# Kernel tuning notes

Hardware: AMD Instinct MI355X
Metric: run time of the kernel (lower is better)

## Reference

```python
import jax, jax.numpy as jnp
import numpy as np

VOCAB, EMB, HID, T = 33, 16, 128, 14

def setup_inputs() -> dict:
    key = jax.random.key(0)
    ks = jax.random.split(key, 12)
    B = 131072
    x = jax.random.randint(ks[0], (B, T), 0, VOCAB, dtype=jnp.int32)
    s = 1.0 / np.sqrt(HID)
    emb_table = jax.random.normal(ks[1], (VOCAB, EMB), dtype=jnp.float32)
    # torch LSTM params: gate order [i, f, g, o], uniform(-1/sqrt(H), 1/sqrt(H))
    W_ih = jax.random.uniform(ks[2], (4 * HID, EMB), minval=-s, maxval=s, dtype=jnp.float32)
    W_hh = jax.random.uniform(ks[3], (4 * HID, HID), minval=-s, maxval=s, dtype=jnp.float32)
    b_ih = jax.random.uniform(ks[4], (4 * HID,), minval=-s, maxval=s, dtype=jnp.float32)
    b_hh = jax.random.uniform(ks[5], (4 * HID,), minval=-s, maxval=s, dtype=jnp.float32)
    W1 = jax.random.uniform(ks[6], (64, 128), minval=-s, maxval=s, dtype=jnp.float32)
    b1 = jax.random.uniform(ks[7], (64,), minval=-s, maxval=s, dtype=jnp.float32)
    W2 = jax.random.uniform(ks[8], (32, 64), minval=-0.125, maxval=0.125, dtype=jnp.float32)
    b2 = jax.random.uniform(ks[9], (32,), minval=-0.125, maxval=0.125, dtype=jnp.float32)
    W3 = jax.random.uniform(ks[10], (2, 32), minval=-0.176, maxval=0.176, dtype=jnp.float32)
    b3 = jax.random.uniform(ks[11], (2,), minval=-0.176, maxval=0.176, dtype=jnp.float32)
    return {"x": x, "emb_table": emb_table, "W_ih": W_ih, "W_hh": W_hh,
            "b_ih": b_ih, "b_hh": b_hh, "W1": W1, "b1": b1,
            "W2": W2, "b2": b2, "W3": W3, "b3": b3}

def reference(x, emb_table, W_ih, W_hh, b_ih, b_hh, W1, b1, W2, b2, W3, b3):
    B = x.shape[0]
    # padding_idx=0: row 0 is zero
    table = emb_table.at[0].set(0.0)
    emb = table[x]                                # [B, T, E]
    # precompute input projections for all timesteps in one GEMM
    x_proj = jnp.einsum('bte,ge->btg', emb, W_ih) + b_ih + b_hh  # [B, T, 4H]

    def step(carry, xp_t):
        h, c = carry
        gates = xp_t + h @ W_hh.T                 # [B, 4H]
        i, f, g, o = jnp.split(gates, 4, axis=-1)
        i, f, o = jax.nn.sigmoid(i), jax.nn.sigmoid(f), jax.nn.sigmoid(o)
        g = jnp.tanh(g)
        c = f * c + i * g
        h = o * jnp.tanh(c)
        return (h, c), None

    h0 = jnp.zeros((B, HID), dtype=emb.dtype)
    c0 = jnp.zeros((B, HID), dtype=emb.dtype)
    (h_last, _), _ = jax.lax.scan(step, (h0, c0), jnp.swapaxes(x_proj, 0, 1))

    y = jax.nn.sigmoid(h_last @ W1.T + b1)
    y = jax.nn.sigmoid(y @ W2.T + b2)
    return y @ W3.T + b3                          # [B, 2]
```

## Files before the change

### kernel.cpp

```cpp
#include <hip/hip_runtime.h>
#include <hip/hip_bf16.h>

#define TSTEP 14
#define BROWS 128
#define KCOMB 160
#define ESTR  16
#define L2E   1.4426950408889634f
#define L2E2  2.8853900817779268f

typedef __attribute__((ext_vector_type(8))) short bf16x8;
typedef __attribute__((ext_vector_type(4))) float f32x4;
typedef __attribute__((ext_vector_type(4))) int   i32x4;

#define MFMA(a,b,c) __builtin_amdgcn_mfma_f32_16x16x32_bf16((a),(b),(c),0,0,0)

__device__ inline ushort f2b(float f){
  union { float f; unsigned u; } v; v.f = f;
  unsigned r = v.u + 0x7fff + ((v.u >> 16) & 1);
  return (ushort)(r >> 16);
}
__device__ inline float rcpf(float x){ return __builtin_amdgcn_rcpf(x); }

#if __has_builtin(__builtin_amdgcn_exp2f)
__device__ inline float EXP2(float x){ return __builtin_amdgcn_exp2f(x); }
#else
__device__ inline float EXP2(float x){ return __expf(x * 0.6931471805599453f); }
#endif

__device__ inline unsigned cvt_pk_bf16(float lo, float hi){
  unsigned r;
  asm("v_cvt_pk_bf16_f32 %0, %1, %2" : "=v"(r) : "v"(lo), "v"(hi));
  return r;
}

__global__ void prep_kernel(const float* __restrict__ W_ih, const float* __restrict__ W_hh,
                            const float* __restrict__ W1,   const float* __restrict__ W2,
                            ushort* __restrict__ wcomb, ushort* __restrict__ w1b, ushort* __restrict__ w2b){
  int i = blockIdx.x * blockDim.x + threadIdx.x;
  if (i < 512*KCOMB){
    int n = i / KCOMB, k = i - n*KCOMB;
    float s = ((n >> 7) == 2) ? L2E2 : L2E;
    float v = (k < 128) ? W_hh[n*128 + k]*s : ((k < 144) ? W_ih[n*16 + (k-128)]*s : 0.f);
    wcomb[i] = f2b(v);
  } else if (i < 512*KCOMB + 64*128){
    int j = i - 512*KCOMB;
    w1b[j] = f2b(W1[j] * L2E);
  } else if (i < 512*KCOMB + 64*128 + 32*64){
    int j = i - 512*KCOMB - 64*128;
    w2b[j] = f2b(W2[j] * L2E);
  }
}

__global__ __attribute__((amdgpu_flat_work_group_size(512, 512), amdgpu_waves_per_eu(2, 2)))
void lstm_kernel(const int* __restrict__ x, const float* __restrict__ emb_table,
                 const float* __restrict__ b_ih, const float* __restrict__ b_hh,
                 const float* __restrict__ b1, const float* __restrict__ b2,
                 const float* __restrict__ W3, const float* __restrict__ b3,
                 const ushort* __restrict__ wcomb, const ushort* __restrict__ w1b,
                 const ushort* __restrict__ w2b, float* __restrict__ out)
{
  __shared__ ushort A_h[2*2*64*128];
  __shared__ __align__(16) char Ebuf[2*TSTEP*64*ESTR*2];

  ushort* E  = (ushort*)Ebuf;
  ushort* y1 = (ushort*)Ebuf;
  float*  y2 = (float*)(Ebuf + 16384);

  const int tid  = threadIdx.x;
  const int lane = tid & 63;
  const int w    = tid >> 6;
  const int l15  = lane & 15;
  const int lg   = lane >> 4;
  const int r0   = blockIdx.x * BROWS;

  { i32x4* az = (i32x4*)A_h;
    #pragma unroll
    for (int i = 0; i < 2; ++i){
      az[tid + i*512]        = (i32x4){0,0,0,0};
      az[2048 + tid + i*512] = (i32x4){0,0,0,0};
    } }

  for (int idx = tid; idx < BROWS*TSTEP; idx += 512){
    int r = idx / TSTEP, t = idx - r*TSTEP;
    int tok = x[(r0 + r)*TSTEP + t];
    int tt = r >> 6, rr = r & 63;
    int xr  = (rr >> 2) & 1;
    unsigned* dst = (unsigned*)(E + tt*(TSTEP*64*ESTR) + (t*64 + rr)*ESTR);
    if (tok == 0){
      #pragma unroll
      for (int e = 0; e < 8; ++e) dst[e] = 0u;
    } else {
      const float* src = emb_table + tok*16;
      #pragma unroll
      for (int e = 0; e < 8; ++e)
        dst[((e >> 2) ^ xr)*4 + (e & 3)] = cvt_pk_bf16(src[2*e], src[2*e+1]);
    }
  }

  bf16x8 bB[4][5];
  #pragma unroll
  for (int g = 0; g < 4; ++g){
    const int n = g*128 + w*16 + l15;
    #pragma unroll
    for (int kt = 0; kt < 5; ++kt)
      bB[g][kt] = *(const bf16x8*)((const short*)wcomb + n*KCOMB + kt*32 + lg*8);
  }

  f32x4 biasv[4];
  #pragma unroll
  for (int g = 0; g < 4; ++g){
    const int n = g*128 + w*16 + l15;
    float bv = (b_ih[n] + b_hh[n]) * ((g == 2) ? L2E2 : L2E);
    biasv[g] = (f32x4){bv,bv,bv,bv};
  }

  f32x4 cst[2][4];
  #pragma unroll
  for (int tt = 0; tt < 2; ++tt)
    #pragma unroll
    for (int m = 0; m < 4; ++m) cst[tt][m] = (f32x4){0.f,0.f,0.f,0.f};

  const int j2 = w*16 + l15;

  __syncthreads();

  for (int t = 0; t < TSTEP; ++t){
    const int bufR = t & 1, bufW = bufR ^ 1;

    #pragma unroll
    for (int m = 0; m < 4; ++m){
      #pragma unroll
      for (int tt = 0; tt < 2; ++tt){
        const ushort* Ar = A_h + (tt*2 + bufR)*8192;
        ushort*       Aw = A_h + (tt*2 + bufW)*8192;
        const short*  Et = (const short*)E + tt*(TSTEP*64*ESTR) + t*64*ESTR;

        const int row = m*16 + l15;
        const int swz = (row & 7) << 3;
        const short* base_e = (const short*)Ar + row*128 + ((lg*8) ^ swz);
        const short* base_o = (const short*)Ar + row*128 + ((32 + lg*8) ^ swz);
        bf16x8 aF[5];
        aF[0] = *(const bf16x8*)(base_e);
        aF[1] = *(const bf16x8*)(base_o);
        aF[2] = *(const bf16x8*)(base_e + 64);
        aF[3] = *(const bf16x8*)(base_o + 64);
        aF[4] = *(const bf16x8*)(Et + row*ESTR + (((lg & 1) ^ ((row >> 2) & 1))*8));

        f32x4 acc[4];
        #pragma unroll
        for (int g = 0; g < 4; ++g){
          acc[g] = MFMA(aF[0], bB[g][0], biasv[g]);
          #pragma unroll
          for (int kt = 1; kt < 5; ++kt)
            acc[g] = MFMA(aF[kt], bB[g][kt], acc[g]);
        }

        #pragma unroll
        for (int rp = 0; rp < 2; ++rp){
          float h2[2];
          #pragma unroll
          for (int q = 0; q < 2; ++q){
            const int r = rp*2 + q;
            float iv = rcpf(1.f + EXP2(-acc[0][r]));
            float fv = rcpf(1.f + EXP2(-acc[1][r]));
            float gv = __builtin_fmaf(-2.f, rcpf(EXP2(acc[2][r]) + 1.f), 1.f);
            float ov = rcpf(1.f + EXP2(-acc[3][r]));
            float cv = __builtin_fmaf(fv, cst[tt][m][r], iv*gv);
            cst[tt][m][r] = cv;
            h2[q] = ov * __builtin_fmaf(-2.f, rcpf(EXP2(cv*L2E2) + 1.f), 1.f);
          }
          unsigned u = cvt_pk_bf16(h2[0], h2[1]);
          const int row0 = m*16 + lg*4 + rp*2;
          const int row1 = row0 + 1;
          Aw[row0*128 + (j2 ^ ((row0 & 7) << 3))] = (ushort)u;
          Aw[row1*128 + (j2 ^ ((row1 & 7) << 3))] = (ushort)(u >> 16);
        }
      }
    }

    __syncthreads();
  }


  {
    f32x4 acc1[4];
    #pragma unroll
    for (int nt = 0; nt < 4; ++nt){
      float bv = b1[nt*16 + l15] * L2E;
      acc1[nt] = (f32x4){bv,bv,bv,bv};
    }
    const int arowg = w*16 + l15;
    const ushort* Hf = A_h + ((w >> 2)*2 + 0)*8192;
    const int arow = arowg & 63;
    const int aswz = (arow & 7) << 3;
    const short* abase = (const short*)Hf + arow*128;
    #pragma unroll
    for (int kt = 0; kt < 4; ++kt){
      bf16x8 aF = *(const bf16x8*)(abase + ((kt*32 + lg*8) ^ aswz));
      #pragma unroll
      for (int nt = 0; nt < 4; ++nt){
        const int n = nt*16 + l15;
        bf16x8 bF = *(const bf16x8*)((const short*)w1b + n*128 + kt*32 + lg*8);
        acc1[nt] = MFMA(aF, bF, acc1[nt]);
      }
    }
    #pragma unroll
    for (int nt = 0; nt < 4; ++nt)
      #pragma unroll
      for (int r = 0; r < 4; ++r){
        const int row = w*16 + lg*4 + r;
        const int col = nt*16 + l15;
        y1[row*64 + (col ^ ((row & 7) << 3))] = f2b(rcpf(1.f + EXP2(-acc1[nt][r])));
      }
  }
  __syncthreads();

  {
    f32x4 acc2[2];
    #pragma unroll
    for (int nt = 0; nt < 2; ++nt){
      float bv = b2[nt*16 + l15] * L2E;
      acc2[nt] = (f32x4){bv,bv,bv,bv};
    }
    const int arow = w*16 + l15;
    const int aswz = (arow & 7) << 3;
    const short* abase = (const short*)y1 + arow*64;
    #pragma unroll
    for (int kt = 0; kt < 2; ++kt){
      bf16x8 aF = *(const bf16x8*)(abase + ((kt*32 + lg*8) ^ aswz));
      #pragma unroll
      for (int nt = 0; nt < 2; ++nt){
        const int n = nt*16 + l15;
        bf16x8 bF = *(const bf16x8*)((const short*)w2b + n*64 + kt*32 + lg*8);
        acc2[nt] = MFMA(aF, bF, acc2[nt]);
      }
    }
    #pragma unroll
    for (int nt = 0; nt < 2; ++nt)
      #pragma unroll
      for (int r = 0; r < 4; ++r){
        const int row = w*16 + lg*4 + r;
        const int col = nt*16 + l15;
        y2[row*33 + col] = rcpf(1.f + EXP2(-acc2[nt][r]));
      }
  }
  __syncthreads();

  if (tid < 256){
    const int lr = tid >> 1, oc = tid & 1;
    float s = b3[oc];
    #pragma unroll
    for (int k = 0; k < 32; ++k)
      s += y2[lr*33 + k] * W3[oc*32 + k];
    out[(size_t)(r0 + lr)*2 + oc] = s;
  }
}

extern "C" void kernel_launch(void* const* d_in, const int* in_sizes, int n_in,
                              void* d_out, int out_size, void* d_ws, size_t ws_size,
                              hipStream_t stream){
  const int*   x    = (const int*)  d_in[0];
  const float* emb  = (const float*)d_in[1];
  const float* W_ih = (const float*)d_in[2];
  const float* W_hh = (const float*)d_in[3];
  const float* b_ih = (const float*)d_in[4];
  const float* b_hh = (const float*)d_in[5];
  const float* W1   = (const float*)d_in[6];
  const float* b1   = (const float*)d_in[7];
  const float* W2   = (const float*)d_in[8];
  const float* b2   = (const float*)d_in[9];
  const float* W3   = (const float*)d_in[10];
  const float* b3   = (const float*)d_in[11];
  float* out = (float*)d_out;

  const int B = in_sizes[0] / TSTEP;

  ushort* wcomb = (ushort*)d_ws;
  ushort* w1b   = wcomb + 512*KCOMB;
  ushort* w2b   = w1b + 64*128;

  const int prep_total = 512*KCOMB + 64*128 + 32*64;
  prep_kernel<<<(prep_total + 255)/256, 256, 0, stream>>>(W_ih, W_hh, W1, W2, wcomb, w1b, w2b);
  lstm_kernel<<<B/BROWS, 512, 0, stream>>>(x, emb, b_ih, b_hh, b1, b2, W3, b3,
                                           wcomb, w1b, w2b, out);
}
```

Baseline: 363.7 us.

## Transpose LSTM MFMA operands, software-pipeline matmul with activations, fuse gate math

The MFMA operands are swapped so each lane's accumulator holds four consecutive hidden units of a single batch row. This lets the new h values be written to LDS as one 8-byte store instead of scattered 2-byte stores. The step loop is restructured so the MFMA group for the next tile is issued before the activation of the previous tile, interleaving matrix and transcendental work. The gate activations are rewritten algebraically so the cell update shares one reciprocal across i, f and g, and h needs only one more reciprocal. This cuts reciprocal count but adds register pressure and slightly different rounding.

Measured after the change: 333.9 us. 1.09x faster.

```diff
diff --git a/kernel.cpp b/kernel.cpp
--- a/kernel.cpp
+++ b/kernel.cpp
@@ -51,6 +51,49 @@
   }
 }
 
+__device__ __forceinline__ void lm_group(const ushort* Ar, const short* Et, int n,
+    int l15, int o0, int o1, int o2, int o3, int esel,
+    const bf16x8 (&bB)[4][5], const f32x4 (&bias)[4], f32x4 (&acc)[4])
+{
+  const short* base = (const short*)Ar + n*2048 + l15*128;
+  bf16x8 a0 = *(const bf16x8*)(base + o0);
+  bf16x8 a1 = *(const bf16x8*)(base + o1);
+  bf16x8 a2 = *(const bf16x8*)(base + o2);
+  bf16x8 a3 = *(const bf16x8*)(base + o3);
+  bf16x8 a4 = *(const bf16x8*)(Et + n*16*ESTR + l15*ESTR + esel);
+  #pragma unroll
+  for (int g = 0; g < 4; ++g){
+    acc[g] = MFMA(bB[g][0], a0, bias[g]);
+    acc[g] = MFMA(bB[g][1], a1, acc[g]);
+    acc[g] = MFMA(bB[g][2], a2, acc[g]);
+    acc[g] = MFMA(bB[g][3], a3, acc[g]);
+    acc[g] = MFMA(bB[g][4], a4, acc[g]);
+  }
+}
+
+__device__ __forceinline__ void act_group(ushort* Aw, int n, int l15, int colswz,
+    const f32x4 (&acc)[4], f32x4 &c)
+{
+  float h2[4];
+  #pragma unroll
+  for (int r = 0; r < 4; ++r){
+    float Aa = EXP2(-acc[0][r]);
+    float Ff = EXP2(-acc[1][r]);
+    float Bb = EXP2( acc[2][r]);
+    float A1 = 1.f + Aa, F1 = 1.f + Ff, Bp = Bb + 1.f, Bm = Bb - 1.f;
+    float P  = A1 * Bp;
+    float cv = __builtin_fmaf(c[r], P, Bm*F1) * rcpf(P*F1);
+    c[r] = cv;
+    float Oo = EXP2(-acc[3][r]);
+    float Ee = EXP2(cv*L2E2);
+    h2[r] = (Ee - 1.f) * rcpf((1.f + Oo)*(Ee + 1.f));
+  }
+  unsigned u0 = cvt_pk_bf16(h2[0], h2[1]);
+  unsigned u1 = cvt_pk_bf16(h2[2], h2[3]);
+  uint2 uu; uu.x = u0; uu.y = u1;
+  *(uint2*)(Aw + n*2048 + l15*128 + colswz) = uu;
+}
+
 __global__ __attribute__((amdgpu_flat_work_group_size(512, 512), amdgpu_waves_per_eu(2, 2)))
 void lstm_kernel(const int* __restrict__ x, const float* __restrict__ emb_table,
                  const float* __restrict__ b_ih, const float* __restrict__ b_hh,
@@ -81,7 +124,7 @@
     } }
 
   for (int idx = tid; idx < BROWS*TSTEP; idx += 512){
-    int r = idx / TSTEP, t = idx - r*TSTEP;
+    int r = idx & 127, t = idx >> 7;
     int tok = x[(r0 + r)*TSTEP + t];
     int tt = r >> 6, rr = r & 63;
     int xr  = (rr >> 2) & 1;
@@ -109,74 +152,55 @@
   f32x4 biasv[4];
   #pragma unroll
   for (int g = 0; g < 4; ++g){
-    const int n = g*128 + w*16 + l15;
-    float bv = (b_ih[n] + b_hh[n]) * ((g == 2) ? L2E2 : L2E);
-    biasv[g] = (f32x4){bv,bv,bv,bv};
+    #pragma unroll
+    for (int r = 0; r < 4; ++r){
+      const int n = g*128 + w*16 + lg*4 + r;
+      biasv[g][r] = (b_ih[n] + b_hh[n]) * ((g == 2) ? L2E2 : L2E);
+    }
   }
 
   f32x4 cst[2][4];
   #pragma unroll
   for (int tt = 0; tt < 2; ++tt)
     #pragma unroll
-    for (int m = 0; m < 4; ++m) cst[tt][m] = (f32x4){0.f,0.f,0.f,0.f};
-
-  const int j2 = w*16 + l15;
+    for (int n = 0; n < 4; ++n) cst[tt][n] = (f32x4){0.f,0.f,0.f,0.f};
+
+  const int sw   = (l15 & 7) << 3;
+  const int o0   = (0*32 + lg*8) ^ sw;
+  const int o1   = (1*32 + lg*8) ^ sw;
+  const int o2   = (2*32 + lg*8) ^ sw;
+  const int o3   = (3*32 + lg*8) ^ sw;
+  const int esel = ((lg & 1) ^ ((l15 >> 2) & 1)) * 8;
+  const int colswz = (w*16 + lg*4) ^ sw;
 
   __syncthreads();
 
   for (int t = 0; t < TSTEP; ++t){
     const int bufR = t & 1, bufW = bufR ^ 1;
-
-    #pragma unroll
-    for (int m = 0; m < 4; ++m){
-      #pragma unroll
-      for (int tt = 0; tt < 2; ++tt){
-        const ushort* Ar = A_h + (tt*2 + bufR)*8192;
-        ushort*       Aw = A_h + (tt*2 + bufW)*8192;
-        const short*  Et = (const short*)E + tt*(TSTEP*64*ESTR) + t*64*ESTR;
-
-        const int row = m*16 + l15;
-        const int swz = (row & 7) << 3;
-        const short* base_e = (const short*)Ar + row*128 + ((lg*8) ^ swz);
-        const short* base_o = (const short*)Ar + row*128 + ((32 + lg*8) ^ swz);
-        bf16x8 aF[5];
-        aF[0] = *(const bf16x8*)(base_e);
-        aF[1] = *(const bf16x8*)(base_o);
-        aF[2] = *(const bf16x8*)(base_e + 64);
-        aF[3] = *(const bf16x8*)(base_o + 64);
-        aF[4] = *(const bf16x8*)(Et + row*ESTR + (((lg & 1) ^ ((row >> 2) & 1))*8));
-
-        f32x4 acc[4];
-        #pragma unroll
-        for (int g = 0; g < 4; ++g){
-          acc[g] = MFMA(aF[0], bB[g][0], biasv[g]);
-          #pragma unroll
-          for (int kt = 1; kt < 5; ++kt)
-            acc[g] = MFMA(aF[kt], bB[g][kt], acc[g]);
-        }
-
-        #pragma unroll
-        for (int rp = 0; rp < 2; ++rp){
-          float h2[2];
-          #pragma unroll
-          for (int q = 0; q < 2; ++q){
-            const int r = rp*2 + q;
-            float iv = rcpf(1.f + EXP2(-acc[0][r]));
-            float fv = rcpf(1.f + EXP2(-acc[1][r]));
-            float gv = __builtin_fmaf(-2.f, rcpf(EXP2(acc[2][r]) + 1.f), 1.f);
-            float ov = rcpf(1.f + EXP2(-acc[3][r]));
-            float cv = __builtin_fmaf(fv, cst[tt][m][r], iv*gv);
-            cst[tt][m][r] = cv;
-            h2[q] = ov * __builtin_fmaf(-2.f, rcpf(EXP2(cv*L2E2) + 1.f), 1.f);
-          }
-          unsigned u = cvt_pk_bf16(h2[0], h2[1]);
-          const int row0 = m*16 + lg*4 + rp*2;
-          const int row1 = row0 + 1;
-          Aw[row0*128 + (j2 ^ ((row0 & 7) << 3))] = (ushort)u;
-          Aw[row1*128 + (j2 ^ ((row1 & 7) << 3))] = (ushort)(u >> 16);
-        }
-      }
-    }
+    const ushort* Ar0 = A_h + bufR*8192;
+    const ushort* Ar1 = A_h + 16384 + bufR*8192;
+    ushort*       Aw0 = A_h + bufW*8192;
+    ushort*       Aw1 = A_h + 16384 + bufW*8192;
+    const short*  Et0 = (const short*)E + t*64*ESTR;
+    const short*  Et1 = (const short*)E + TSTEP*64*ESTR + t*64*ESTR;
+
+    f32x4 accA[4], accB[4];
+    lm_group(Ar0, Et0, 0, l15, o0,o1,o2,o3, esel, bB, biasv, accA);
+    lm_group(Ar0, Et0, 1, l15, o0,o1,o2,o3, esel, bB, biasv, accB);
+    act_group(Aw0, 0, l15, colswz, accA, cst[0][0]);
+    lm_group(Ar0, Et0, 2, l15, o0,o1,o2,o3, esel, bB, biasv, accA);
+    act_group(Aw0, 1, l15, colswz, accB, cst[0][1]);
+    lm_group(Ar0, Et0, 3, l15, o0,o1,o2,o3, esel, bB, biasv, accB);
+    act_group(Aw0, 2, l15, colswz, accA, cst[0][2]);
+    lm_group(Ar1, Et1, 0, l15, o0,o1,o2,o3, esel, bB, biasv, accA);
+    act_group(Aw0, 3, l15, colswz, accB, cst[0][3]);
+    lm_group(Ar1, Et1, 1, l15, o0,o1,o2,o3, esel, bB, biasv, accB);
+    act_group(Aw1, 0, l15, colswz, accA, cst[1][0]);
+    lm_group(Ar1, Et1, 2, l15, o0,o1,o2,o3, esel, bB, biasv, accA);
+    act_group(Aw1, 1, l15, colswz, accB, cst[1][1]);
+    lm_group(Ar1, Et1, 3, l15, o0,o1,o2,o3, esel, bB, biasv, accB);
+    act_group(Aw1, 2, l15, colswz, accA, cst[1][2]);
+    act_group(Aw1, 3, l15, colswz, accB, cst[1][3]);
 
     __syncthreads();
   }
@@ -189,9 +213,8 @@
       float bv = b1[nt*16 + l15] * L2E;
       acc1[nt] = (f32x4){bv,bv,bv,bv};
     }
-    const int arowg = w*16 + l15;
-    const ushort* Hf = A_h + ((w >> 2)*2 + 0)*8192;
-    const int arow = arowg & 63;
+    const ushort* Hf = A_h + (w >> 2)*16384;
+    const int arow = (w*16 + l15) & 63;
     const int aswz = (arow & 7) << 3;
     const short* abase = (const short*)Hf + arow*128;
     #pragma unroll
```
